# Kernel tuning notes

Hardware: AMD Instinct MI355X
Metric: run time of the kernel (lower is better)

## Reference

```python
import jax, jax.numpy as jnp
import numpy as np

EMBED_DIM = 512
N_HEAD = 8
HEAD_DIM = EMBED_DIM // N_HEAD  # 64
B, S = 2, 4096
NEG_FILL = -1e20


def setup_inputs() -> dict:
    key = jax.random.key(0)
    ks = jax.random.split(key, 9)
    inp = {
        "key": jax.random.normal(ks[0], (B, S, EMBED_DIM), jnp.float32),
        "query": jax.random.normal(ks[1], (B, S, EMBED_DIM), jnp.float32),
        "value": jax.random.normal(ks[2], (B, S, EMBED_DIM), jnp.float32),
        "mask": jax.random.randint(ks[3], (1, 1, S, S), 0, 2, jnp.int32),
        # per-head projections (shared across heads, as in the source: a single
        # d x d nn.Linear applied to the last dim of [B,S,H,d])
        "Wq": jax.random.normal(ks[4], (HEAD_DIM, HEAD_DIM), jnp.float32) / np.sqrt(HEAD_DIM),
        "Wk": jax.random.normal(ks[5], (HEAD_DIM, HEAD_DIM), jnp.float32) / np.sqrt(HEAD_DIM),
        "Wv": jax.random.normal(ks[6], (HEAD_DIM, HEAD_DIM), jnp.float32) / np.sqrt(HEAD_DIM),
        "Wo": jax.random.normal(ks[7], (EMBED_DIM, EMBED_DIM), jnp.float32) / np.sqrt(EMBED_DIM),
        "bo": jax.random.normal(ks[8], (EMBED_DIM,), jnp.float32) * 0.01,
    }
    return inp


def reference(key, query, value, mask, Wq, Wk, Wv, Wo, bo):
    b, sq, e = query.shape
    skv = key.shape[1]
    h, d = N_HEAD, HEAD_DIM
    # split heads: [B, S, H, d]
    q = query.reshape(b, sq, h, d) @ Wq.T
    k = key.reshape(b, skv, h, d) @ Wk.T
    v = value.reshape(b, skv, h, d) @ Wv.T
    # scores: [B, H, Sq, Skv]
    scores = jnp.einsum("bqhd,bkhd->bhqk", q, k)
    # source masks BEFORE scaling: fill -1e20 then divide by sqrt(d)
    scores = jnp.where(mask == 0, NEG_FILL, scores)
    scores = scores / np.sqrt(d).astype(np.float32)
    attn = jax.nn.softmax(scores, axis=-1)
    ctx = jnp.einsum("bhqk,bkhd->bqhd", attn, v)  # [B, Sq, H, d]
    concat = ctx.reshape(b, sq, h * d)
    return concat @ Wo.T + bo
```

## Files before the change

### kernel.cpp

```cpp
#include <hip/hip_runtime.h>

typedef __bf16 bf16;
typedef __attribute__((ext_vector_type(8)))  bf16     bf16x8;
typedef __attribute__((ext_vector_type(4)))  bf16     bf16x4;
typedef __attribute__((ext_vector_type(16))) float    f32x16;
typedef __attribute__((ext_vector_type(4)))  float    f32x4;
typedef __attribute__((ext_vector_type(4)))  unsigned uint4v;
typedef __attribute__((ext_vector_type(2)))  unsigned uint2v;

#define SLEN 4096
#define HDIM 64
#define EMB 512
#define NTILES 64
#define SCALE_LOG2E 0.1803336100254854f

__device__ __forceinline__ f32x16 mfma32(bf16x8 a, bf16x8 b, f32x16 c) {
  return __builtin_amdgcn_mfma_f32_32x32x16_bf16(a, b, c, 0, 0, 0);
}

__device__ __forceinline__ void cp16(const void* g, const void* l) {
  __builtin_amdgcn_global_load_lds(
      (__attribute__((address_space(1))) unsigned int*)(unsigned long long)g,
      (__attribute__((address_space(3))) unsigned int*)(unsigned int)(unsigned long long)l,
      16, 0, 0);
}

__device__ __forceinline__ unsigned pk2(float a, float b) {
  unsigned short ua = __builtin_bit_cast(unsigned short, (bf16)a);
  unsigned short ub = __builtin_bit_cast(unsigned short, (bf16)b);
  return (unsigned)ua | ((unsigned)ub << 16);
}

__global__ __launch_bounds__(256, 2) void proj_qkv(
    const float* __restrict__ key, const float* __restrict__ query, const float* __restrict__ value,
    const float* __restrict__ Wq, const float* __restrict__ Wk, const float* __restrict__ Wv,
    bf16* __restrict__ Qb, bf16* __restrict__ Kb, bf16* __restrict__ VT)
{
  __shared__ __align__(16) bf16 tile[128][64];
  const int tid = threadIdx.x, w = tid >> 6, lane = tid & 63, l31 = lane & 31, lh = lane >> 5;
  const int r0 = blockIdx.x * 128;
  const int m0 = r0 + w * 32;

  #pragma unroll
  for (int p = 0; p < 3; ++p) {
    const float* X = (p == 0) ? query : (p == 1) ? key : value;
    const float* W = (p == 0) ? Wq    : (p == 1) ? Wk  : Wv;

    bf16x8 af[4];
    {
      const float* xr = X + (size_t)(m0 + l31) * 64 + 8 * lh;
      #pragma unroll
      for (int c = 0; c < 4; ++c) {
        f32x4 lo = *(const f32x4*)(xr + c * 16);
        f32x4 hi = *(const f32x4*)(xr + c * 16 + 4);
        bf16x8 v;
        #pragma unroll
        for (int j = 0; j < 4; ++j) { v[j] = (bf16)lo[j]; v[4 + j] = (bf16)hi[j]; }
        af[c] = v;
      }
    }
    bf16x8 bfr[2][4];
    #pragma unroll
    for (int nb = 0; nb < 2; ++nb) {
      const float* wr = W + (size_t)(l31 + 32 * nb) * 64 + 8 * lh;
      #pragma unroll
      for (int c = 0; c < 4; ++c) {
        f32x4 lo = *(const f32x4*)(wr + c * 16);
        f32x4 hi = *(const f32x4*)(wr + c * 16 + 4);
        bf16x8 v;
        #pragma unroll
        for (int j = 0; j < 4; ++j) { v[j] = (bf16)lo[j]; v[4 + j] = (bf16)hi[j]; }
        bfr[nb][c] = v;
      }
    }
    f32x16 a0, a1;
    #pragma unroll
    for (int r = 0; r < 16; ++r) { a0[r] = 0.f; a1[r] = 0.f; }
    #pragma unroll
    for (int c = 0; c < 4; ++c) {
      a0 = mfma32(af[c], bfr[0][c], a0);
      a1 = mfma32(af[c], bfr[1][c], a1);
    }

    const float qs = (p == 0) ? SCALE_LOG2E : 1.0f;
    __syncthreads();
    #pragma unroll
    for (int r = 0; r < 16; ++r) {
      const int row = w * 32 + (r & 3) + 8 * (r >> 2) + 4 * lh;
      tile[row][l31]      = (bf16)(a0[r] * qs);
      tile[row][l31 + 32] = (bf16)(a1[r] * qs);
    }
    __syncthreads();

    if (p < 2) {
      bf16* OUT = p ? Kb : Qb;
      const int rloc = tid >> 1, hf = tid & 1;
      const int rg = r0 + rloc, bs = rg >> 3, h = rg & 7, b = bs >> 12, sidx = bs & 4095;
      bf16* dst = OUT + (((size_t)(b * 8 + h) * SLEN + sidx) * 64 + hf * 32);
      const bf16* srcp = &tile[rloc][hf * 32];
      #pragma unroll
      for (int u = 0; u < 4; ++u) *(uint4v*)(dst + u * 8) = *(const uint4v*)(srcp + u * 8);
    } else {
      const int h = tid >> 5, d0 = tid & 31;
      const int b = blockIdx.x >> 8, s0 = (blockIdx.x * 16) & 4095;
      #pragma unroll
      for (int dh = 0; dh < 2; ++dh) {
        const int dd = d0 + 32 * dh;
        unsigned pk4[8];
        #pragma unroll
        for (int t2 = 0; t2 < 8; ++t2) {
          unsigned short ua = __builtin_bit_cast(unsigned short, tile[(2 * t2) * 8 + h][dd]);
          unsigned short ub = __builtin_bit_cast(unsigned short, tile[(2 * t2 + 1) * 8 + h][dd]);
          pk4[t2] = (unsigned)ua | ((unsigned)ub << 16);
        }
        bf16* dst = VT + ((size_t)(b * 8 + h) * 64 + dd) * SLEN + s0;
        uint4v A; A[0] = pk4[0]; A[1] = pk4[1]; A[2] = pk4[2]; A[3] = pk4[3];
        uint4v Bv; Bv[0] = pk4[4]; Bv[1] = pk4[5]; Bv[2] = pk4[6]; Bv[3] = pk4[7];
        *(uint4v*)(dst) = A;
        *(uint4v*)(dst + 8) = Bv;
      }
    }
  }
}

__device__ __forceinline__ unsigned nib_compress(unsigned x) {
  x = (x | (x >> 4)) & 0x00FF00FFu;
  x = (x | (x >> 8)) & 0x0000FFFFu;
  return x;
}
__global__ void pack_mask(const int* __restrict__ mask, unsigned* __restrict__ MW)
{
  const int w = threadIdx.x >> 6, lane = threadIdx.x & 63;
  const int q = blockIdx.x * 4 + w;
  const int* row = mask + (size_t)q * SLEN;
  unsigned long long mine = 0ull;
  #pragma unroll 4
  for (int i = 0; i < 64; ++i) {
    unsigned long long b = __ballot(row[i * 64 + lane] != 0);
    if (i == lane) mine = b;
  }
  const unsigned lo = (unsigned)mine, hi = (unsigned)(mine >> 32);
  const unsigned w0 = nib_compress(lo & 0x0F0F0F0Fu)        | (nib_compress(hi & 0x0F0F0F0Fu) << 16);
  const unsigned w1 = nib_compress((lo >> 4) & 0x0F0F0F0Fu) | (nib_compress((hi >> 4) & 0x0F0F0F0Fu) << 16);
  MW[(size_t)lane * SLEN + q] = w0;
  MW[(size_t)NTILES * SLEN + (size_t)lane * SLEN + q] = w1;
}

__global__ void wo_split(const float* __restrict__ Wo, bf16* __restrict__ WH, bf16* __restrict__ WL)
{
  const int i = (blockIdx.x * 256 + threadIdx.x) * 4;
  f32x4 v = *(const f32x4*)(Wo + i);
  bf16x4 h, l;
  #pragma unroll
  for (int j = 0; j < 4; ++j) { h[j] = (bf16)v[j]; l[j] = (bf16)(v[j] - (float)h[j]); }
  *(bf16x4*)(WH + i) = h;
  *(bf16x4*)(WL + i) = l;
}

__global__ __launch_bounds__(256, 4) void attn_kernel(
    const bf16* __restrict__ Qb, const bf16* __restrict__ Kb, const bf16* __restrict__ VT,
    const unsigned* __restrict__ MW,
    bf16* __restrict__ ctxh, bf16* __restrict__ ctxl,
    float* __restrict__ PO, float* __restrict__ PLg, int split)
{
  __shared__ __align__(16) unsigned char smem[32768];
  unsigned char* const Ksm = smem;
  unsigned char* const Vsm = smem + 16384;

  const int tid = threadIdx.x, w = tid >> 6, lane = tid & 63, l31 = lane & 31, lh = lane >> 5;
  const int qg = w & 1, kc = w >> 1;
  const int half = blockIdx.x >> 10;
  const int rem = blockIdx.x & 1023;
  const int bh = rem >> 6, qt = rem & 63;
  const int q0 = qt * 64;
  const int qrow = q0 + qg * 32 + l31;
  const int lh4 = 4 * lh;
  const int kcs = kc << 4;
  const int ntiles = (split == 2) ? 32 : 64;
  const int kt0 = half * 32;

  const bf16* qp = Qb + ((size_t)bh * SLEN + qrow) * HDIM + 8 * lh;
  const bf16x8 qf0 = *(const bf16x8*)(qp);
  const bf16x8 qf1 = *(const bf16x8*)(qp + 16);
  const bf16x8 qf2 = *(const bf16x8*)(qp + 32);
  const bf16x8 qf3 = *(const bf16x8*)(qp + 48);

  const int f0 = 2 * w, f1 = 2 * w + 1;
  const bf16* kp0 = Kb + ((size_t)bh * SLEN + kt0 * 64 + (f0 >> 2) * 32 + l31) * HDIM + (f0 & 3) * 16 + 8 * lh;
  const bf16* kp1 = Kb + ((size_t)bh * SLEN + kt0 * 64 + (f1 >> 2) * 32 + l31) * HDIM + (f1 & 3) * 16 + 8 * lh;
  const bf16* vp0 = VT + ((size_t)bh * HDIM + (f0 >> 2) * 32 + l31) * SLEN + kt0 * 64 + (f0 & 3) * 16 + 8 * lh;
  const bf16* vp1 = VT + ((size_t)bh * HDIM + (f1 >> 2) * 32 + l31) * SLEN + kt0 * 64 + (f1 & 3) * 16 + 8 * lh;
  unsigned char* const dk0 = Ksm + f0 * 1024;
  unsigned char* const dv0 = Vsm + f0 * 1024;

  const int lb = lane * 16;
  const unsigned char* kr = Ksm + kc * 4096 + lb;
  const unsigned char* vr = Vsm + kc * 2048 + lb;

  f32x16 o0, o1, Z16;
  #pragma unroll
  for (int r = 0; r < 16; ++r) { o0[r] = 0.f; o1[r] = 0.f; Z16[r] = 0.f; }
  float la0 = 0.f, la1 = 0.f, la2 = 0.f, la3 = 0.f;

  cp16(kp0, dk0); cp16(kp1, dk0 + 1024); cp16(vp0, dv0); cp16(vp1, dv0 + 1024);
  kp0 += 4096; kp1 += 4096; vp0 += 64; vp1 += 64;
  const unsigned* mp = MW + (size_t)lh * NTILES * SLEN + (size_t)kt0 * SLEN + qrow;
  unsigned mwc = *mp;
  __syncthreads();

#define LDK(B, C)      (*(const bf16x8*)(kr + (B) * 8192 + (C) * 1024))
#define LDV(B, MB, CC) (*(const bf16x8*)(vr + (B) * 8192 + (MB) * 4096 + (CC) * 1024))

#define TILE(B, MWCUR, MWNXT) { \
  MWNXT = mp[SLEN]; mp += SLEN; \
  cp16(kp0, dk0 + (1 - (B)) * 8192); cp16(kp1, dk0 + (1 - (B)) * 8192 + 1024); \
  cp16(vp0, dv0 + (1 - (B)) * 8192); cp16(vp1, dv0 + (1 - (B)) * 8192 + 1024); \
  kp0 += 4096; kp1 += 4096; vp0 += 64; vp1 += 64; \
  f32x16 s = mfma32(LDK(B, 0), qf0, Z16); \
  s = mfma32(LDK(B, 1), qf1, s); \
  s = mfma32(LDK(B, 2), qf2, s); \
  s = mfma32(LDK(B, 3), qf3, s); \
  const unsigned mwk = (MWCUR) >> kcs; \
  float p[16]; \
  _Pragma("unroll") \
  for (int r = 0; r < 16; ++r) { \
    float e = __builtin_amdgcn_exp2f(s[r]); \
    unsigned kbit = (unsigned)(((int)(mwk << (31 - r))) >> 31); \
    e = __builtin_bit_cast(float, __builtin_bit_cast(unsigned, e) & kbit); \
    p[r] = e; \
    if ((r & 3) == 0) la0 += e; else if ((r & 3) == 1) la1 += e; \
    else if ((r & 3) == 2) la2 += e; else la3 += e; \
  } \
  _Pragma("unroll") \
  for (int b = 0; b < 2; ++b) { \
    unsigned Wa = pk2(p[8 * b + 0], p[8 * b + 1]); \
    unsigned Wb = pk2(p[8 * b + 2], p[8 * b + 3]); \
    unsigned Wc = pk2(p[8 * b + 4], p[8 * b + 5]); \
    unsigned Wd = pk2(p[8 * b + 6], p[8 * b + 7]); \
    uint2v s02 = __builtin_amdgcn_permlane32_swap(Wa, Wc, false, false); \
    uint2v s13 = __builtin_amdgcn_permlane32_swap(Wb, Wd, false, false); \
    uint4v fw; fw[0] = s02[0]; fw[1] = s13[0]; fw[2] = s02[1]; fw[3] = s13[1]; \
    const bf16x8 bp = __builtin_bit_cast(bf16x8, fw); \
    o0 = mfma32(LDV(B, 0, b), bp, o0); \
    o1 = mfma32(LDV(B, 1, b), bp, o1); \
  } \
  __syncthreads(); \
}

  const int pairs = ntiles >> 1;
  unsigned mwn;
  for (int tp = 0; tp < pairs; ++tp) {
    TILE(0, mwc, mwn)
    TILE(1, mwn, mwc)
  }
#undef LDK
#undef LDV
#undef TILE

  float plsum = (la0 + la1) + (la2 + la3);
  plsum += __shfl_xor(plsum, 32);

  float* POl = (float*)smem;
  float* PLl = (float*)(smem + 16384);

  if (w >= 2) {
    const int pw = w - 2;
    #pragma unroll
    for (int r = 0; r < 16; ++r) {
      POl[(pw * 32 + r) * 64 + lane]      = o0[r];
      POl[(pw * 32 + 16 + r) * 64 + lane] = o1[r];
    }
    PLl[pw * 64 + lane] = plsum;
  }
  __syncthreads();
  if (w < 2) {
    #pragma unroll
    for (int r = 0; r < 16; ++r) {
      o0[r] += POl[(w * 32 + r) * 64 + lane];
      o1[r] += POl[(w * 32 + 16 + r) * 64 + lane];
    }
    plsum += PLl[w * 64 + lane];
  }

  if (split == 1) {
    if (w < 2) {
      const float inv = 1.f / plsum;
      #pragma unroll
      for (int r = 0; r < 16; ++r) { o0[r] *= inv; o1[r] *= inv; }
    }
    __syncthreads();

    bf16* Tr = (bf16*)(smem + 17408);
    if (w < 2) {
      #pragma unroll
      for (int r = 0; r < 16; ++r) {
        const int dr = (r & 3) + 8 * (r >> 2) + lh4;
        Tr[(w * 32 + l31) * 72 + dr]      = (bf16)o0[r];
        Tr[(w * 32 + l31) * 72 + 32 + dr] = (bf16)o1[r];
      }
    }
    __syncthreads();
    if (tid < 128) {
      const int rloc = tid >> 1, hf = tid & 1;
      bf16* dst = ctxh + ((size_t)bh * SLEN + q0 + rloc) * 64 + hf * 32;
      const bf16* srcp = Tr + rloc * 72 + hf * 32;
      #pragma unroll
      for (int u = 0; u < 4; ++u) *(uint4v*)(dst + u * 8) = *(const uint4v*)(srcp + u * 8);
    }
    __syncthreads();
    if (w < 2) {
      #pragma unroll
      for (int r = 0; r < 16; ++r) {
        const int dr = (r & 3) + 8 * (r >> 2) + lh4;
        const float h0 = (float)(bf16)o0[r];
        const float h1 = (float)(bf16)o1[r];
        Tr[(w * 32 + l31) * 72 + dr]      = (bf16)(o0[r] - h0);
        Tr[(w * 32 + l31) * 72 + 32 + dr] = (bf16)(o1[r] - h1);
      }
    }
    __syncthreads();
    if (tid < 128) {
      const int rloc = tid >> 1, hf = tid & 1;
      bf16* dst = ctxl + ((size_t)bh * SLEN + q0 + rloc) * 64 + hf * 32;
      const bf16* srcp = Tr + rloc * 72 + hf * 32;
      #pragma unroll
      for (int u = 0; u < 4; ++u) *(uint4v*)(dst + u * 8) = *(const uint4v*)(srcp + u * 8);
    }
  } else {
    __syncthreads();
    float* Trf = (float*)smem;
    float* PLs = (float*)(smem + 17408);
    if (w < 2) {
      #pragma unroll
      for (int r = 0; r < 16; ++r) {
        const int dr = (r & 3) + 8 * (r >> 2) + lh4;
        Trf[(w * 32 + l31) * 68 + dr]      = o0[r];
        Trf[(w * 32 + l31) * 68 + 32 + dr] = o1[r];
      }
      if (lh == 0) PLs[w * 32 + l31] = plsum;
    }
    __syncthreads();
    const int qq = tid >> 2, part = tid & 3;
    float* dst = PO + ((size_t)(half * 16 + bh) * SLEN + q0 + qq) * 64 + part * 16;
    const float* srcp = Trf + qq * 68 + part * 16;
    #pragma unroll
    for (int u = 0; u < 4; ++u) *(f32x4*)(dst + u * 4) = *(const f32x4*)(srcp + u * 4);
    if (tid < 64) PLg[(size_t)(half * 16 + bh) * SLEN + q0 + tid] = PLs[tid];
  }
}

__global__ __launch_bounds__(256) void combine_halves(
    const float* __restrict__ PO, const float* __restrict__ PLg,
    bf16* __restrict__ CH, bf16* __restrict__ CL)
{
  const int bh = blockIdx.x >> 5, qt = blockIdx.x & 31;
  const int t = threadIdx.x;
  const int q = qt * 128 + (t >> 1);
  const size_t HOFF = (size_t)16 * SLEN * 64;
  const size_t base = ((size_t)bh * SLEN + q) * 64 + (t & 1) * 32;
  const float inv = 1.f / (PLg[(size_t)bh * SLEN + q] +
                           PLg[(size_t)16 * SLEN + (size_t)bh * SLEN + q]);
  const float* p0 = PO + base;
  const float* p1 = PO + HOFF + base;
  unsigned hw[16], lw[16];
  #pragma unroll
  for (int i = 0; i < 8; ++i) {
    f32x4 a = *(const f32x4*)(p0 + i * 4);
    f32x4 b = *(const f32x4*)(p1 + i * 4);
    float v0 = (a[0] + b[0]) * inv, v1 = (a[1] + b[1]) * inv;
    float v2 = (a[2] + b[2]) * inv, v3 = (a[3] + b[3]) * inv;
    float h0 = (float)(bf16)v0, h1 = (float)(bf16)v1;
    float h2 = (float)(bf16)v2, h3 = (float)(bf16)v3;
    hw[i * 2]     = pk2(v0, v1);
    hw[i * 2 + 1] = pk2(v2, v3);
    lw[i * 2]     = pk2(v0 - h0, v1 - h1);
    lw[i * 2 + 1] = pk2(v2 - h2, v3 - h3);
  }
  bf16* ch = CH + base;
  bf16* cl = CL + base;
  #pragma unroll
  for (int u = 0; u < 4; ++u) {
    uint4v H; H[0] = hw[u*4]; H[1] = hw[u*4+1]; H[2] = hw[u*4+2]; H[3] = hw[u*4+3];
    uint4v L; L[0] = lw[u*4]; L[1] = lw[u*4+1]; L[2] = lw[u*4+2]; L[3] = lw[u*4+3];
    *(uint4v*)(ch + u * 8) = H;
    *(uint4v*)(cl + u * 8) = L;
  }
}

__global__ __launch_bounds__(256, 2) void out_proj(
    const bf16* __restrict__ CH, const bf16* __restrict__ CL,
    const bf16* __restrict__ WH, const bf16* __restrict__ WL,
    const float* __restrict__ bo, float* __restrict__ out)
{
  __shared__ __align__(16) bf16 Af[2][4][4][64][8];
  const int tid = threadIdx.x, w = tid >> 6, lane = tid & 63, l31 = lane & 31, lh = lane >> 5;
  const int mt = blockIdx.x >> 3, nt = blockIdx.x & 7;
  const int bs0 = mt * 128, n0 = nt * 64;
  const int b = bs0 >> 12, sbase = bs0 & 4095;

  f32x16 a0, a1;
  #pragma unroll
  for (int r = 0; r < 16; ++r) { a0[r] = 0.f; a1[r] = 0.f; }

  for (int kk = 0; kk < 8; ++kk) {
    __syncthreads();
    #pragma unroll
    for (int qq = 0; qq < 8; ++qq) {
      const int fid = w * 8 + qq, pl = fid >> 4, mb = (fid >> 2) & 3, c = fid & 3;
      const bf16* src = (pl ? CL : CH) +
          ((size_t)(b * 8 + kk) * SLEN + sbase + 32 * mb + l31) * 64 + 16 * c + 8 * lh;
      cp16(src, &Af[pl][mb][c][0][0]);
    }
    __syncthreads();

    bf16x8 bh0[4], bl0[4], bh1[4], bl1[4], ah[4], al[4];
    #pragma unroll
    for (int c = 0; c < 4; ++c) {
      const size_t o0off = (size_t)(n0 + l31) * EMB + kk * 64 + 16 * c + 8 * lh;
      const size_t o1off = (size_t)(n0 + l31 + 32) * EMB + kk * 64 + 16 * c + 8 * lh;
      bh0[c] = *(const bf16x8*)(WH + o0off);
      bl0[c] = *(const bf16x8*)(WL + o0off);
      bh1[c] = *(const bf16x8*)(WH + o1off);
      bl1[c] = *(const bf16x8*)(WL + o1off);
      ah[c] = *(const bf16x8*)(&Af[0][w][c][lane][0]);
      al[c] = *(const bf16x8*)(&Af[1][w][c][lane][0]);
    }
    #pragma unroll
    for (int c = 0; c < 4; ++c) {
      a0 = mfma32(ah[c], bh0[c], a0);
      a0 = mfma32(ah[c], bl0[c], a0);
      a0 = mfma32(al[c], bh0[c], a0);
      a1 = mfma32(ah[c], bh1[c], a1);
      a1 = mfma32(ah[c], bl1[c], a1);
      a1 = mfma32(al[c], bh1[c], a1);
    }
  }

  const float bv0 = bo[n0 + l31], bv1 = bo[n0 + l31 + 32];
  #pragma unroll
  for (int r = 0; r < 16; ++r) {
    const int row = bs0 + w * 32 + (r & 3) + 8 * (r >> 2) + 4 * lh;
    out[(size_t)row * EMB + n0 + l31]      = a0[r] + bv0;
    out[(size_t)row * EMB + n0 + l31 + 32] = a1[r] + bv1;
  }
}

extern "C" void kernel_launch(void* const* d_in, const int* in_sizes, int n_in,
                              void* d_out, int out_size, void* d_ws, size_t ws_size,
                              hipStream_t stream)
{
  (void)in_sizes; (void)n_in; (void)out_size;
  const float* key   = (const float*)d_in[0];
  const float* query = (const float*)d_in[1];
  const float* value = (const float*)d_in[2];
  const int*   mask  = (const int*)d_in[3];
  const float* Wq    = (const float*)d_in[4];
  const float* Wk    = (const float*)d_in[5];
  const float* Wv    = (const float*)d_in[6];
  const float* Wo    = (const float*)d_in[7];
  const float* bo    = (const float*)d_in[8];
  float* out = (float*)d_out;

  char* ws = (char*)d_ws;
  bf16* Qb = (bf16*)(ws);
  bf16* Kb = (bf16*)(ws + (8ull  << 20));
  bf16* VT = (bf16*)(ws + (16ull << 20));
  unsigned* MW = (unsigned*)(ws + (24ull << 20));
  bf16* CH = (bf16*)(ws + (26ull << 20));
  bf16* CL = (bf16*)(ws + (34ull << 20));
  bf16* WH = (bf16*)(ws + (42ull << 20));
  bf16* WL = (bf16*)(ws + (42ull << 20) + (512ull << 10));
  float* PO  = (float*)(ws + (44ull << 20));
  float* PLg = (float*)(ws + (78ull << 20));

  const size_t need_split = (78ull << 20) + (2ull * 16 * SLEN * 4);
  const int split = (ws_size >= need_split) ? 2 : 1;

  proj_qkv<<<512, 256, 0, stream>>>(key, query, value, Wq, Wk, Wv, Qb, Kb, VT);
  pack_mask<<<1024, 256, 0, stream>>>(mask, MW);
  wo_split<<<256, 256, 0, stream>>>(Wo, WH, WL);
  attn_kernel<<<1024 * split, 256, 0, stream>>>(Qb, Kb, VT, MW, CH, CL, PO, PLg, split);
  if (split == 2) combine_halves<<<512, 256, 0, stream>>>(PO, PLg, CH, CL);
  out_proj<<<512, 256, 0, stream>>>(CH, CL, WH, WL, bo, out);
}
```

Baseline: 249.5 us.

## Pre-swizzle K/V into MFMA fragment image and stream per-wave from global

The projection kernel now writes K and V into a combined, pre-tiled image laid out exactly as MFMA fragments, so the attention kernel can load operands straight from global/L2 without an LDS staging buffer or per-tile barriers. Each wave now works on its own 32-query block over half the keys, and the transposed mask words are fetched as vectors. The split-by-workspace fallback is removed, so the two-half partial-output path and the combine kernel always run. This drops the LDS copies and __syncthreads from the inner loop, at the cost of relying on cache hits for K/V reuse across waves and losing block-level data sharing.

```diff
diff --git a/kernel.cpp b/kernel.cpp
--- a/kernel.cpp
+++ b/kernel.cpp
@@ -11,7 +11,6 @@
 #define SLEN 4096
 #define HDIM 64
 #define EMB 512
-#define NTILES 64
 #define SCALE_LOG2E 0.1803336100254854f
 
 __device__ __forceinline__ f32x16 mfma32(bf16x8 a, bf16x8 b, f32x16 c) {
@@ -34,9 +33,9 @@
 __global__ __launch_bounds__(256, 2) void proj_qkv(
     const float* __restrict__ key, const float* __restrict__ query, const float* __restrict__ value,
     const float* __restrict__ Wq, const float* __restrict__ Wk, const float* __restrict__ Wv,
-    bf16* __restrict__ Qb, bf16* __restrict__ Kb, bf16* __restrict__ VT)
-{
-  __shared__ __align__(16) bf16 tile[128][64];
+    bf16* __restrict__ Qb, char* __restrict__ KV)
+{
+  __shared__ __align__(16) bf16 tile[128][72];
   const int tid = threadIdx.x, w = tid >> 6, lane = tid & 63, l31 = lane & 31, lh = lane >> 5;
   const int r0 = blockIdx.x * 128;
   const int m0 = r0 + w * 32;
@@ -92,32 +91,48 @@
     }
     __syncthreads();
 
-    if (p < 2) {
-      bf16* OUT = p ? Kb : Qb;
+    if (p == 0) {
       const int rloc = tid >> 1, hf = tid & 1;
       const int rg = r0 + rloc, bs = rg >> 3, h = rg & 7, b = bs >> 12, sidx = bs & 4095;
-      bf16* dst = OUT + (((size_t)(b * 8 + h) * SLEN + sidx) * 64 + hf * 32);
+      bf16* dst = Qb + (((size_t)(b * 8 + h) * SLEN + sidx) * 64 + hf * 32);
       const bf16* srcp = &tile[rloc][hf * 32];
       #pragma unroll
       for (int u = 0; u < 4; ++u) *(uint4v*)(dst + u * 8) = *(const uint4v*)(srcp + u * 8);
+    } else if (p == 1) {
+      const int b = blockIdx.x >> 8;
+      const int s0 = (blockIdx.x & 255) * 16;
+      #pragma unroll
+      for (int u = 0; u < 4; ++u) {
+        const int pid = u * 256 + tid;
+        const int sl = pid & 15, h = (pid >> 4) & 7, plh = (pid >> 7) & 1, c = pid >> 8;
+        const int s = s0 + sl;
+        const int bh = b * 8 + h, hf2 = s >> 11, tt = (s >> 5) & 63, kl = s & 31;
+        char* dst = KV + ((size_t)((bh * 2 + hf2) * 64 + tt) * 8192)
+                       + c * 1024 + (kl + 32 * plh) * 16;
+        *(uint4v*)dst = *(const uint4v*)&tile[sl * 8 + h][c * 16 + plh * 8];
+      }
     } else {
-      const int h = tid >> 5, d0 = tid & 31;
-      const int b = blockIdx.x >> 8, s0 = (blockIdx.x * 16) & 4095;
+      const int b = blockIdx.x >> 8;
+      const int s0 = (blockIdx.x & 255) * 16;
+      const int cc = (s0 >> 4) & 1;
+      const int hf2 = s0 >> 11, tt = (s0 >> 5) & 63;
       #pragma unroll
-      for (int dh = 0; dh < 2; ++dh) {
-        const int dd = d0 + 32 * dh;
-        unsigned pk4[8];
+      for (int u = 0; u < 4; ++u) {
+        const int pid = u * 256 + tid;
+        const int ld = pid & 31, db = (pid >> 5) & 1, plh = (pid >> 6) & 1, h = pid >> 7;
+        const int d = db * 32 + ld;
+        const int bh = b * 8 + h;
+        unsigned wds[4];
         #pragma unroll
-        for (int t2 = 0; t2 < 8; ++t2) {
-          unsigned short ua = __builtin_bit_cast(unsigned short, tile[(2 * t2) * 8 + h][dd]);
-          unsigned short ub = __builtin_bit_cast(unsigned short, tile[(2 * t2 + 1) * 8 + h][dd]);
-          pk4[t2] = (unsigned)ua | ((unsigned)ub << 16);
+        for (int t2 = 0; t2 < 4; ++t2) {
+          unsigned short ua = __builtin_bit_cast(unsigned short, tile[(plh * 8 + 2 * t2) * 8 + h][d]);
+          unsigned short ub = __builtin_bit_cast(unsigned short, tile[(plh * 8 + 2 * t2 + 1) * 8 + h][d]);
+          wds[t2] = (unsigned)ua | ((unsigned)ub << 16);
         }
-        bf16* dst = VT + ((size_t)(b * 8 + h) * 64 + dd) * SLEN + s0;
-        uint4v A; A[0] = pk4[0]; A[1] = pk4[1]; A[2] = pk4[2]; A[3] = pk4[3];
-        uint4v Bv; Bv[0] = pk4[4]; Bv[1] = pk4[5]; Bv[2] = pk4[6]; Bv[3] = pk4[7];
-        *(uint4v*)(dst) = A;
-        *(uint4v*)(dst + 8) = Bv;
+        char* dst = KV + ((size_t)((bh * 2 + hf2) * 64 + tt) * 8192) + 4096
+                       + (db * 2 + cc) * 1024 + (ld + 32 * plh) * 16;
+        uint4v A; A[0] = wds[0]; A[1] = wds[1]; A[2] = wds[2]; A[3] = wds[3];
+        *(uint4v*)dst = A;
       }
     }
   }
@@ -128,7 +143,7 @@
   x = (x | (x >> 8)) & 0x0000FFFFu;
   return x;
 }
-__global__ void pack_mask(const int* __restrict__ mask, unsigned* __restrict__ MW)
+__global__ void pack_mask(const int* __restrict__ mask, unsigned* __restrict__ MT)
 {
   const int w = threadIdx.x >> 6, lane = threadIdx.x & 63;
   const int q = blockIdx.x * 4 + w;
@@ -142,8 +157,8 @@
   const unsigned lo = (unsigned)mine, hi = (unsigned)(mine >> 32);
   const unsigned w0 = nib_compress(lo & 0x0F0F0F0Fu)        | (nib_compress(hi & 0x0F0F0F0Fu) << 16);
   const unsigned w1 = nib_compress((lo >> 4) & 0x0F0F0F0Fu) | (nib_compress((hi >> 4) & 0x0F0F0F0Fu) << 16);
-  MW[(size_t)lane * SLEN + q] = w0;
-  MW[(size_t)NTILES * SLEN + (size_t)lane * SLEN + q] = w1;
+  MT[((size_t)q) * 64 + lane] = w0;
+  MT[((size_t)(4096 + q)) * 64 + lane] = w1;
 }
 
 __global__ void wo_split(const float* __restrict__ Wo, bf16* __restrict__ WH, bf16* __restrict__ WL)
@@ -158,26 +173,16 @@
 }
 
 __global__ __launch_bounds__(256, 4) void attn_kernel(
-    const bf16* __restrict__ Qb, const bf16* __restrict__ Kb, const bf16* __restrict__ VT,
-    const unsigned* __restrict__ MW,
-    bf16* __restrict__ ctxh, bf16* __restrict__ ctxl,
-    float* __restrict__ PO, float* __restrict__ PLg, int split)
-{
-  __shared__ __align__(16) unsigned char smem[32768];
-  unsigned char* const Ksm = smem;
-  unsigned char* const Vsm = smem + 16384;
+    const bf16* __restrict__ Qb, const char* __restrict__ KV, const unsigned* __restrict__ MT,
+    float* __restrict__ PO, float* __restrict__ PLg)
+{
+  __shared__ __align__(16) unsigned char smem[4][8448];
 
   const int tid = threadIdx.x, w = tid >> 6, lane = tid & 63, l31 = lane & 31, lh = lane >> 5;
-  const int qg = w & 1, kc = w >> 1;
-  const int half = blockIdx.x >> 10;
-  const int rem = blockIdx.x & 1023;
-  const int bh = rem >> 6, qt = rem & 63;
-  const int q0 = qt * 64;
-  const int qrow = q0 + qg * 32 + l31;
-  const int lh4 = 4 * lh;
-  const int kcs = kc << 4;
-  const int ntiles = (split == 2) ? 32 : 64;
-  const int kt0 = half * 32;
+  const int wid = blockIdx.x * 4 + w;
+  const int qt = wid & 127, bh = (wid >> 7) & 15, half = wid >> 11;
+  const int q0w = qt * 32;
+  const int qrow = q0w + l31;
 
   const bf16* qp = Qb + ((size_t)bh * SLEN + qrow) * HDIM + 8 * lh;
   const bf16x8 qf0 = *(const bf16x8*)(qp);
@@ -185,168 +190,92 @@
   const bf16x8 qf2 = *(const bf16x8*)(qp + 32);
   const bf16x8 qf3 = *(const bf16x8*)(qp + 48);
 
-  const int f0 = 2 * w, f1 = 2 * w + 1;
-  const bf16* kp0 = Kb + ((size_t)bh * SLEN + kt0 * 64 + (f0 >> 2) * 32 + l31) * HDIM + (f0 & 3) * 16 + 8 * lh;
-  const bf16* kp1 = Kb + ((size_t)bh * SLEN + kt0 * 64 + (f1 >> 2) * 32 + l31) * HDIM + (f1 & 3) * 16 + 8 * lh;
-  const bf16* vp0 = VT + ((size_t)bh * HDIM + (f0 >> 2) * 32 + l31) * SLEN + kt0 * 64 + (f0 & 3) * 16 + 8 * lh;
-  const bf16* vp1 = VT + ((size_t)bh * HDIM + (f1 >> 2) * 32 + l31) * SLEN + kt0 * 64 + (f1 & 3) * 16 + 8 * lh;
-  unsigned char* const dk0 = Ksm + f0 * 1024;
-  unsigned char* const dv0 = Vsm + f0 * 1024;
-
-  const int lb = lane * 16;
-  const unsigned char* kr = Ksm + kc * 4096 + lb;
-  const unsigned char* vr = Vsm + kc * 2048 + lb;
-
-  f32x16 o0, o1, Z16;
-  #pragma unroll
-  for (int r = 0; r < 16; ++r) { o0[r] = 0.f; o1[r] = 0.f; Z16[r] = 0.f; }
+  const char* kb = KV + ((size_t)((bh * 2 + half) * 64) * 8192);
+  {
+    unsigned long long ka = (unsigned long long)kb;
+    unsigned lo_ = __builtin_amdgcn_readfirstlane((unsigned)ka);
+    unsigned hi_ = __builtin_amdgcn_readfirstlane((unsigned)(ka >> 32));
+    kb = (const char*)(((unsigned long long)hi_ << 32) | (unsigned long long)lo_);
+  }
+  const int vo = lane * 16;
+
+  const unsigned* mtp = MT + ((size_t)(lh * 4096 + qrow)) * 64 + half * 32;
+  uint4v mw = *(const uint4v*)(mtp);
+
+  f32x16 o0, o1;
+  #pragma unroll
+  for (int r = 0; r < 16; ++r) { o0[r] = 0.f; o1[r] = 0.f; }
   float la0 = 0.f, la1 = 0.f, la2 = 0.f, la3 = 0.f;
 
-  cp16(kp0, dk0); cp16(kp1, dk0 + 1024); cp16(vp0, dv0); cp16(vp1, dv0 + 1024);
-  kp0 += 4096; kp1 += 4096; vp0 += 64; vp1 += 64;
-  const unsigned* mp = MW + (size_t)lh * NTILES * SLEN + (size_t)kt0 * SLEN + qrow;
-  unsigned mwc = *mp;
-  __syncthreads();
-
-#define LDK(B, C)      (*(const bf16x8*)(kr + (B) * 8192 + (C) * 1024))
-#define LDV(B, MB, CC) (*(const bf16x8*)(vr + (B) * 8192 + (MB) * 4096 + (CC) * 1024))
-
-#define TILE(B, MWCUR, MWNXT) { \
-  MWNXT = mp[SLEN]; mp += SLEN; \
-  cp16(kp0, dk0 + (1 - (B)) * 8192); cp16(kp1, dk0 + (1 - (B)) * 8192 + 1024); \
-  cp16(vp0, dv0 + (1 - (B)) * 8192); cp16(vp1, dv0 + (1 - (B)) * 8192 + 1024); \
-  kp0 += 4096; kp1 += 4096; vp0 += 64; vp1 += 64; \
-  f32x16 s = mfma32(LDK(B, 0), qf0, Z16); \
-  s = mfma32(LDK(B, 1), qf1, s); \
-  s = mfma32(LDK(B, 2), qf2, s); \
-  s = mfma32(LDK(B, 3), qf3, s); \
-  const unsigned mwk = (MWCUR) >> kcs; \
+#define TILE32(WORD, SH) { \
+  const bf16x8 kf0 = *(const bf16x8*)(kb + vo); \
+  const bf16x8 kf1 = *(const bf16x8*)(kb + vo + 1024); \
+  const bf16x8 kf2 = *(const bf16x8*)(kb + vo + 2048); \
+  const bf16x8 kf3 = *(const bf16x8*)(kb + vo + 3072); \
+  const bf16x8 vf0 = *(const bf16x8*)(kb + vo + 4096); \
+  const bf16x8 vf1 = *(const bf16x8*)(kb + vo + 5120); \
+  const bf16x8 vf2 = *(const bf16x8*)(kb + vo + 6144); \
+  const bf16x8 vf3 = *(const bf16x8*)(kb + vo + 7168); \
+  f32x16 s; \
+  _Pragma("unroll") for (int r = 0; r < 16; ++r) s[r] = 0.f; \
+  s = mfma32(kf0, qf0, s); s = mfma32(kf1, qf1, s); \
+  s = mfma32(kf2, qf2, s); s = mfma32(kf3, qf3, s); \
   float p[16]; \
-  _Pragma("unroll") \
-  for (int r = 0; r < 16; ++r) { \
+  _Pragma("unroll") for (int r = 0; r < 16; ++r) { \
     float e = __builtin_amdgcn_exp2f(s[r]); \
-    unsigned kbit = (unsigned)(((int)(mwk << (31 - r))) >> 31); \
+    unsigned kbit = (unsigned)(((int)((WORD) << (31 - (SH) - r))) >> 31); \
     e = __builtin_bit_cast(float, __builtin_bit_cast(unsigned, e) & kbit); \
     p[r] = e; \
     if ((r & 3) == 0) la0 += e; else if ((r & 3) == 1) la1 += e; \
-    else if ((r & 3) == 2) la2 += e; else la3 += e; \
-  } \
-  _Pragma("unroll") \
-  for (int b = 0; b < 2; ++b) { \
-    unsigned Wa = pk2(p[8 * b + 0], p[8 * b + 1]); \
-    unsigned Wb = pk2(p[8 * b + 2], p[8 * b + 3]); \
-    unsigned Wc = pk2(p[8 * b + 4], p[8 * b + 5]); \
-    unsigned Wd = pk2(p[8 * b + 6], p[8 * b + 7]); \
+    else if ((r & 3) == 2) la2 += e; else la3 += e; } \
+  bf16x8 bp0, bp1; \
+  { unsigned Wa = pk2(p[0], p[1]), Wb = pk2(p[2], p[3]); \
+    unsigned Wc = pk2(p[4], p[5]), Wd = pk2(p[6], p[7]); \
     uint2v s02 = __builtin_amdgcn_permlane32_swap(Wa, Wc, false, false); \
     uint2v s13 = __builtin_amdgcn_permlane32_swap(Wb, Wd, false, false); \
     uint4v fw; fw[0] = s02[0]; fw[1] = s13[0]; fw[2] = s02[1]; fw[3] = s13[1]; \
-    const bf16x8 bp = __builtin_bit_cast(bf16x8, fw); \
-    o0 = mfma32(LDV(B, 0, b), bp, o0); \
-    o1 = mfma32(LDV(B, 1, b), bp, o1); \
-  } \
-  __syncthreads(); \
-}
-
-  const int pairs = ntiles >> 1;
-  unsigned mwn;
-  for (int tp = 0; tp < pairs; ++tp) {
-    TILE(0, mwc, mwn)
-    TILE(1, mwn, mwc)
-  }
-#undef LDK
-#undef LDV
-#undef TILE
+    bp0 = __builtin_bit_cast(bf16x8, fw); } \
+  { unsigned Wa = pk2(p[8], p[9]), Wb = pk2(p[10], p[11]); \
+    unsigned Wc = pk2(p[12], p[13]), Wd = pk2(p[14], p[15]); \
+    uint2v s02 = __builtin_amdgcn_permlane32_swap(Wa, Wc, false, false); \
+    uint2v s13 = __builtin_amdgcn_permlane32_swap(Wb, Wd, false, false); \
+    uint4v fw; fw[0] = s02[0]; fw[1] = s13[0]; fw[2] = s02[1]; fw[3] = s13[1]; \
+    bp1 = __builtin_bit_cast(bf16x8, fw); } \
+  o0 = mfma32(vf0, bp0, o0); \
+  o0 = mfma32(vf1, bp1, o0); \
+  o1 = mfma32(vf2, bp0, o1); \
+  o1 = mfma32(vf3, bp1, o1); \
+  kb += 8192; \
+}
+
+  for (int g = 0; g < 8; ++g) {
+    const uint4v mwN = *(const uint4v*)(mtp + 4 * ((g < 7) ? g + 1 : 7));
+    #pragma unroll
+    for (int tp = 0; tp < 4; ++tp) {
+      const unsigned word = mw[tp];
+      TILE32(word, 0)
+      TILE32(word, 16)
+    }
+    mw = mwN;
+  }
+#undef TILE32
 
   float plsum = (la0 + la1) + (la2 + la3);
   plsum += __shfl_xor(plsum, 32);
 
-  float* POl = (float*)smem;
-  float* PLl = (float*)(smem + 16384);
-
-  if (w >= 2) {
-    const int pw = w - 2;
-    #pragma unroll
-    for (int r = 0; r < 16; ++r) {
-      POl[(pw * 32 + r) * 64 + lane]      = o0[r];
-      POl[(pw * 32 + 16 + r) * 64 + lane] = o1[r];
-    }
-    PLl[pw * 64 + lane] = plsum;
-  }
-  __syncthreads();
-  if (w < 2) {
-    #pragma unroll
-    for (int r = 0; r < 16; ++r) {
-      o0[r] += POl[(w * 32 + r) * 64 + lane];
-      o1[r] += POl[(w * 32 + 16 + r) * 64 + lane];
-    }
-    plsum += PLl[w * 64 + lane];
-  }
-
-  if (split == 1) {
-    if (w < 2) {
-      const float inv = 1.f / plsum;
-      #pragma unroll
-      for (int r = 0; r < 16; ++r) { o0[r] *= inv; o1[r] *= inv; }
-    }
-    __syncthreads();
-
-    bf16* Tr = (bf16*)(smem + 17408);
-    if (w < 2) {
-      #pragma unroll
-      for (int r = 0; r < 16; ++r) {
-        const int dr = (r & 3) + 8 * (r >> 2) + lh4;
-        Tr[(w * 32 + l31) * 72 + dr]      = (bf16)o0[r];
-        Tr[(w * 32 + l31) * 72 + 32 + dr] = (bf16)o1[r];
-      }
-    }
-    __syncthreads();
-    if (tid < 128) {
-      const int rloc = tid >> 1, hf = tid & 1;
-      bf16* dst = ctxh + ((size_t)bh * SLEN + q0 + rloc) * 64 + hf * 32;
-      const bf16* srcp = Tr + rloc * 72 + hf * 32;
-      #pragma unroll
-      for (int u = 0; u < 4; ++u) *(uint4v*)(dst + u * 8) = *(const uint4v*)(srcp + u * 8);
-    }
-    __syncthreads();
-    if (w < 2) {
-      #pragma unroll
-      for (int r = 0; r < 16; ++r) {
-        const int dr = (r & 3) + 8 * (r >> 2) + lh4;
-        const float h0 = (float)(bf16)o0[r];
-        const float h1 = (float)(bf16)o1[r];
-        Tr[(w * 32 + l31) * 72 + dr]      = (bf16)(o0[r] - h0);
-        Tr[(w * 32 + l31) * 72 + 32 + dr] = (bf16)(o1[r] - h1);
-      }
-    }
-    __syncthreads();
-    if (tid < 128) {
-      const int rloc = tid >> 1, hf = tid & 1;
-      bf16* dst = ctxl + ((size_t)bh * SLEN + q0 + rloc) * 64 + hf * 32;
-      const bf16* srcp = Tr + rloc * 72 + hf * 32;
-      #pragma unroll
-      for (int u = 0; u < 4; ++u) *(uint4v*)(dst + u * 8) = *(const uint4v*)(srcp + u * 8);
-    }
-  } else {
-    __syncthreads();
-    float* Trf = (float*)smem;
-    float* PLs = (float*)(smem + 17408);
-    if (w < 2) {
-      #pragma unroll
-      for (int r = 0; r < 16; ++r) {
-        const int dr = (r & 3) + 8 * (r >> 2) + lh4;
-        Trf[(w * 32 + l31) * 68 + dr]      = o0[r];
-        Trf[(w * 32 + l31) * 68 + 32 + dr] = o1[r];
-      }
-      if (lh == 0) PLs[w * 32 + l31] = plsum;
-    }
-    __syncthreads();
-    const int qq = tid >> 2, part = tid & 3;
-    float* dst = PO + ((size_t)(half * 16 + bh) * SLEN + q0 + qq) * 64 + part * 16;
-    const float* srcp = Trf + qq * 68 + part * 16;
-    #pragma unroll
-    for (int u = 0; u < 4; ++u) *(f32x4*)(dst + u * 4) = *(const f32x4*)(srcp + u * 4);
-    if (tid < 64) PLg[(size_t)(half * 16 + bh) * SLEN + q0 + tid] = PLs[tid];
-  }
+  float* T = (float*)(smem[w]);
+  #pragma unroll
+  for (int r = 0; r < 16; ++r) {
+    const int dr = (r & 3) + 8 * (r >> 2) + 4 * lh;
+    T[l31 * 65 + dr]      = o0[r];
+    T[l31 * 65 + 32 + dr] = o1[r];
+  }
+  const int q = lane >> 1, side = lane & 1;
+  float* dst = PO + ((size_t)((half * 16 + bh) * SLEN + q0w + q)) * 64 + side * 32;
+  const float* srcp = T + q * 65 + side * 32;
+  #pragma unroll
+  for (int u = 0; u < 8; ++u) *(f32x4*)(dst + u * 4) = *(const f32x4*)(srcp + u * 4);
+  if (lane < 32) PLg[(size_t)(half * 16 + bh) * SLEN + q0w + l31] = plsum;
 }
 
 __global__ __launch_bounds__(256) void combine_halves(
@@ -449,7 +378,7 @@
                               void* d_out, int out_size, void* d_ws, size_t ws_size,
                               hipStream_t stream)
 {
-  (void)in_sizes; (void)n_in; (void)out_size;
+  (void)in_sizes; (void)n_in; (void)out_size; (void)ws_size;
   const float* key   = (const float*)d_in[0];
   const float* query = (const float*)d_in[1];
   const float* value = (const float*)d_in[2];
@@ -463,9 +392,8 @@
 
   char* ws = (char*)d_ws;
   bf16* Qb = (bf16*)(ws);
-  bf16* Kb = (bf16*)(ws + (8ull  << 20));
-  bf16* VT = (bf16*)(ws + (16ull << 20));
-  unsigned* MW = (unsigned*)(ws + (24ull << 20));
+  char* KVimg = ws + (8ull << 20);
+  unsigned* MT = (unsigned*)(ws + (24ull << 20));
   bf16* CH = (bf16*)(ws + (26ull << 20));
   bf16* CL = (bf16*)(ws + (34ull << 20));
   bf16* WH = (bf16*)(ws + (42ull << 20));
@@ -473,13 +401,10 @@
   float* PO  = (float*)(ws + (44ull << 20));
   float* PLg = (float*)(ws + (78ull << 20));
 
-  const size_t need_split = (78ull << 20) + (2ull * 16 * SLEN * 4);
-  const int split = (ws_size >= need_split) ? 2 : 1;
-
-  proj_qkv<<<512, 256, 0, stream>>>(key, query, value, Wq, Wk, Wv, Qb, Kb, VT);
-  pack_mask<<<1024, 256, 0, stream>>>(mask, MW);
+  proj_qkv<<<512, 256, 0, stream>>>(key, query, value, Wq, Wk, Wv, Qb, KVimg);
+  pack_mask<<<1024, 256, 0, stream>>>(mask, MT);
   wo_split<<<256, 256, 0, stream>>>(Wo, WH, WL);
-  attn_kernel<<<1024 * split, 256, 0, stream>>>(Qb, Kb, VT, MW, CH, CL, PO, PLg, split);
-  if (split == 2) combine_halves<<<512, 256, 0, stream>>>(PO, PLg, CH, CL);
+  attn_kernel<<<1024, 256, 0, stream>>>(Qb, KVimg, MT, PO, PLg);
+  combine_halves<<<512, 256, 0, stream>>>(PO, PLg, CH, CL);
   out_proj<<<512, 256, 0, stream>>>(CH, CL, WH, WL, bo, out);
 }
```

Result: slower. 469.8 us (+88.3%).
